# Performance work log

Hardware: AMD Instinct MI355X
Metric: run time of the kernel (lower is better)

## Reference

```python
import jax, jax.numpy as jnp
import numpy as np

B, N, C = 4, 32768, 3          # batch, proposals per sample, classes
PRE, POST = 4096, 512          # NMS_PRE_MAXSIZE, NMS_POST_MAXSIZE
THRESH = 0.7                   # NMS_THRESH


def setup_inputs() -> dict:
    key = jax.random.key(0)
    k1, k2, k3, k4 = jax.random.split(key, 4)
    # realistic 3D boxes: centers in a ~70m range, sizes 1-5m, heading in (-pi, pi)
    centers = jax.random.uniform(k1, (B, N, 3), minval=-35.0, maxval=35.0)
    sizes = jax.random.uniform(k2, (B, N, 3), minval=1.0, maxval=5.0)
    heading = jax.random.uniform(k3, (B, N, 1), minval=-np.pi, maxval=np.pi)
    batch_box_preds = jnp.concatenate([centers, sizes, heading], axis=-1)  # (B,N,7)
    batch_cls_preds = jax.random.normal(k4, (B, N, C))                     # (B,N,3)
    return {"batch_box_preds": batch_box_preds, "batch_cls_preds": batch_cls_preds}


def _bev_iou(boxes):
    # boxes: (K, 7) = (x, y, z, dx, dy, dz, ry); axis-aligned BEV IoU -> (K, K)
    x, y, dx, dy = boxes[:, 0], boxes[:, 1], boxes[:, 3], boxes[:, 4]
    x1, x2 = x - dx * 0.5, x + dx * 0.5
    y1, y2 = y - dy * 0.5, y + dy * 0.5
    iw = jnp.clip(jnp.minimum(x2[:, None], x2[None, :]) - jnp.maximum(x1[:, None], x1[None, :]), 0.0)
    ih = jnp.clip(jnp.minimum(y2[:, None], y2[None, :]) - jnp.maximum(y1[:, None], y1[None, :]), 0.0)
    inter = iw * ih
    area = dx * dy
    union = area[:, None] + area[None, :] - inter
    return inter / jnp.maximum(union, 1e-6)


def _nms_one(boxes, cls_preds):
    # boxes: (N, 7), cls_preds: (N, C)
    scores = jnp.max(cls_preds, axis=1)          # per-box max-class score
    labels = jnp.argmax(cls_preds, axis=1)
    top_scores, idx = jax.lax.top_k(scores, PRE)  # score-sorted candidates
    iou = _bev_iou(boxes[idx])                    # (PRE, PRE)
    ar = jnp.arange(PRE)

    def body(i, keep):
        # suppress later boxes overlapping a still-kept box i
        suppress = (iou[i] > THRESH) & keep[i] & (ar > i)
        return keep & (~suppress)

    keep = jax.lax.fori_loop(0, PRE, body, jnp.ones(PRE, dtype=bool))

    # take first POST kept (already score-ordered); pad with zeros like torch new_zeros buffers
    _, sel_local = jax.lax.top_k(jnp.where(keep, top_scores, -jnp.inf), POST)
    valid = keep[sel_local]
    sel = idx[sel_local]
    rois = jnp.where(valid[:, None], boxes[sel], 0.0)            # (POST, 7)
    roi_scores = jnp.where(valid, scores[sel], 0.0)              # (POST,)
    roi_labels = jnp.where(valid, labels[sel], 0) + 1            # (POST,), +1 as in proposal_layer
    return rois, roi_scores, roi_labels


def reference(batch_box_preds, batch_cls_preds):
    rois, roi_scores, roi_labels = jax.vmap(_nms_one)(batch_box_preds, batch_cls_preds)
    return rois, roi_scores, roi_labels
```

## Files before the change

### kernel.cpp

```cpp
#include <hip/hip_runtime.h>
#include <cstdint>
#include <cstddef>

#define BB 4
#define NN 32768
#define PRE 4096
#define POST 512
#define NW 64
#define PSEL 1024
#define PREF_CH 16

typedef unsigned long long u64;
typedef unsigned int u32;

#define SW(i) ((i) ^ (((i) >> 4) & 15))

__device__ __forceinline__ u32 enc_f32(float f) {
  u32 u = __float_as_uint(f);
  u32 m = (u32)((int)u >> 31) | 0x80000000u;
  return u ^ m;
}

__global__ void score_kernel(const float* __restrict__ cls,
                             float* __restrict__ scores, int* __restrict__ labels) {
  int g = blockIdx.x * blockDim.x + threadIdx.x;
  if (g >= BB * NN) return;
  const float* p = cls + (size_t)g * 3;
  float c0 = p[0], c1 = p[1], c2 = p[2];
  float m = c0; int l = 0;
  if (c1 > m) { m = c1; l = 1; }
  if (c2 > m) { m = c2; l = 2; }
  scores[g] = m;
  labels[g] = l;
}

template<int SELN, bool GATED>
__global__ __launch_bounds__(1024) void select_kernel_t(
    const float* __restrict__ scores, const float* __restrict__ boxes,
    const int* __restrict__ st_info,
    int* __restrict__ top_idx, float* __restrict__ top_score,
    float* __restrict__ bx1, float* __restrict__ bx2,
    float* __restrict__ by1, float* __restrict__ by2, float* __restrict__ bar) {
  constexpr bool HY = (SELN == PSEL);
  int b = blockIdx.x;
  if (GATED && st_info[b * 2 + 0] >= POST) return;
  int tid = threadIdx.x;
  int wv = tid >> 6;
  const float* sc = scores + (size_t)b * NN;

  __shared__ u32 hist16[16][256];
  __shared__ u32 sA[256], sB[256];
  __shared__ u32 scanbuf[1024];
  __shared__ u64 sortbuf[SELN];
  __shared__ u32 sh_prefix;
  __shared__ int sh_rem;

  const int e0 = tid * 32;
  u32 encs[32];
  {
    const float4* sc4 = (const float4*)(sc + e0);
#pragma unroll
    for (int k = 0; k < 8; ++k) {
      float4 v = sc4[k];
      encs[k * 4 + 0] = enc_f32(v.x);
      encs[k * 4 + 1] = enc_f32(v.y);
      encs[k * 4 + 2] = enc_f32(v.z);
      encs[k * 4 + 3] = enc_f32(v.w);
    }
  }

  u32 prefix = 0, known = 0;
  int remaining = SELN;
  for (int shift = 24; shift >= 0; shift -= 8) {
    for (int k = tid; k < 16 * 256; k += 1024) ((u32*)hist16)[k] = 0;
    __syncthreads();
#pragma unroll
    for (int k = 0; k < 32; ++k) {
      u32 u = encs[k];
      if ((u & known) == prefix) atomicAdd(&hist16[wv][(u >> shift) & 255u], 1u);
    }
    __syncthreads();
    if (tid < 256) {
      u32 t = 0;
#pragma unroll
      for (int w2 = 0; w2 < 16; ++w2) t += hist16[w2][tid];
      sA[tid] = t;
    }
    __syncthreads();
    u32* src = sA; u32* dst = sB;
    for (int off = 1; off < 256; off <<= 1) {
      if (tid < 256) dst[tid] = src[tid] + ((tid + off < 256) ? src[tid + off] : 0u);
      __syncthreads();
      u32* tp = src; src = dst; dst = tp;
    }
    if (tid < 256) {
      u32 sv = src[tid];
      u32 svn = (tid < 255) ? src[tid + 1] : 0u;
      if (sv >= (u32)remaining && svn < (u32)remaining) {
        sh_prefix = prefix | ((u32)tid << shift);
        sh_rem = remaining - (int)svn;
      }
    }
    __syncthreads();
    prefix = sh_prefix;
    remaining = sh_rem;
    known |= (0xFFu << shift);
    __syncthreads();
  }
  const u32 pivot = prefix;

  int gtc = 0, eqc = 0;
#pragma unroll
  for (int k = 0; k < 32; ++k) {
    gtc += (encs[k] > pivot);
    eqc += (encs[k] == pivot);
  }
  scanbuf[tid] = ((u32)gtc << 16) | (u32)eqc;
  __syncthreads();
  for (int off = 1; off < 1024; off <<= 1) {
    u32 v = scanbuf[tid];
    u32 add = (tid >= off) ? scanbuf[tid - off] : 0u;
    __syncthreads();
    scanbuf[tid] = v + add;
    __syncthreads();
  }
  u32 incl = scanbuf[tid];
  u32 totpk = scanbuf[1023];
  const int cnt_gt = (int)(totpk >> 16);
  int gt_base = (int)(incl >> 16) - gtc;
  int eq_base = (int)(incl & 0xFFFFu) - eqc;
  int gs = 0, es = 0;
#pragma unroll
  for (int k = 0; k < 32; ++k) {
    u32 u = encs[k];
    int e = e0 + k;
    u64 key = ((u64)u << 32) | (u32)(~(u32)e);
    if (u > pivot) {
      int pos = gt_base + (gs++);
      sortbuf[HY ? pos : SW(pos)] = key;
    } else if (u == pivot) {
      int g = eq_base + (es++);
      if (g < remaining) {
        int pos = cnt_gt + g;
        sortbuf[HY ? pos : SW(pos)] = key;
      }
    }
  }
  __syncthreads();

  if constexpr (HY) {
    u64 key = sortbuf[tid];
#pragma unroll
    for (int k2 = 2; k2 <= 64; k2 <<= 1) {
      for (int j = k2 >> 1; j > 0; j >>= 1) {
        u64 o = __shfl_xor(key, j, 64);
        bool take_max = (((tid & k2) == 0) == ((tid & j) == 0));
        key = ((key > o) == take_max) ? key : o;
      }
    }
    for (int k2 = 128; k2 <= PSEL; k2 <<= 1) {
      for (int j = k2 >> 1; j >= 64; j >>= 1) {
        __syncthreads();
        sortbuf[tid] = key;
        __syncthreads();
        u64 o = sortbuf[tid ^ j];
        bool take_max = (((tid & k2) == 0) == ((tid & j) == 0));
        key = ((key > o) == take_max) ? key : o;
      }
      for (int j = 32; j > 0; j >>= 1) {
        u64 o = __shfl_xor(key, j, 64);
        bool take_max = (((tid & k2) == 0) == ((tid & j) == 0));
        key = ((key > o) == take_max) ? key : o;
      }
    }
    {
#pragma clang fp contract(off)
      int e = (int)(~(u32)(key & 0xFFFFFFFFull));
      top_idx[b * PRE + tid] = e;
      top_score[b * PRE + tid] = sc[e];
      const float* bx = boxes + ((size_t)b * NN + e) * 7;
      float x = bx[0], y = bx[1], dx = bx[3], dy = bx[4];
      float hx = dx * 0.5f, hy = dy * 0.5f;
      bx1[b * PRE + tid] = x - hx;
      bx2[b * PRE + tid] = x + hx;
      by1[b * PRE + tid] = y - hy;
      by2[b * PRE + tid] = y + hy;
      bar[b * PRE + tid] = dx * dy;
    }
  } else {
    for (int k = 2; k <= SELN; k <<= 1) {
      for (int j = k >> 1; j > 0; j >>= 1) {
        for (int p = tid; p < SELN / 2; p += 1024) {
          int low = p & (j - 1);
          int i = ((p ^ low) << 1) | low;
          int ixj = i + j;
          u64 a = sortbuf[SW(i)], c = sortbuf[SW(ixj)];
          bool desc = ((i & k) == 0);
          if (desc ? (a < c) : (a > c)) { sortbuf[SW(i)] = c; sortbuf[SW(ixj)] = a; }
        }
        __syncthreads();
      }
    }
    {
#pragma clang fp contract(off)
      for (int s = tid; s < SELN; s += 1024) {
        u64 key = sortbuf[SW(s)];
        int e = (int)(~(u32)(key & 0xFFFFFFFFull));
        top_idx[b * PRE + s] = e;
        top_score[b * PRE + s] = sc[e];
        const float* bx = boxes + ((size_t)b * NN + e) * 7;
        float x = bx[0], y = bx[1], dx = bx[3], dy = bx[4];
        float hx = dx * 0.5f, hy = dy * 0.5f;
        bx1[b * PRE + s] = x - hx;
        bx2[b * PRE + s] = x + hx;
        by1[b * PRE + s] = y - hy;
        by2[b * PRE + s] = y + hy;
        bar[b * PRE + s] = dx * dy;
      }
    }
  }
}

__device__ __forceinline__ void mask_tile(
    const float* __restrict__ bx1, const float* __restrict__ bx2,
    const float* __restrict__ by1, const float* __restrict__ by2,
    const float* __restrict__ bar, u64* __restrict__ mask,
    int b, int rb, int cb, int t) {
#pragma clang fp contract(off)
  int i = rb * 64 + t;
  int j0 = cb * 64 + t;
  float cx1 = bx1[b * PRE + j0], cx2 = bx2[b * PRE + j0];
  float cy1 = by1[b * PRE + j0], cy2 = by2[b * PRE + j0];
  float car = bar[b * PRE + j0];
  float ix1 = bx1[b * PRE + i], ix2 = bx2[b * PRE + i];
  float iy1 = by1[b * PRE + i], iy2 = by2[b * PRE + i];
  float ia = bar[b * PRE + i];
  u64 bits = 0ull;
  int jbase = cb * 64;
  for (int jj = 0; jj < 64; ++jj) {
    float jx1 = __shfl(cx1, jj, 64);
    float jx2 = __shfl(cx2, jj, 64);
    float jy1 = __shfl(cy1, jj, 64);
    float jy2 = __shfl(cy2, jj, 64);
    float jar = __shfl(car, jj, 64);
    if (jbase + jj > i) {
      float iw = fminf(ix2, jx2) - fmaxf(ix1, jx1);
      iw = fmaxf(iw, 0.0f);
      float ih = fminf(iy2, jy2) - fmaxf(iy1, jy1);
      ih = fmaxf(ih, 0.0f);
      float inter = iw * ih;
      float uni = ia + jar - inter;
      float iou = inter / fmaxf(uni, 1e-6f);
      if (iou > 0.7f) bits |= (1ull << jj);
    }
  }
  mask[((size_t)b * PRE + i) * NW + cb] = bits;
}

__global__ void mask_prefix_kernel(const float* __restrict__ bx1, const float* __restrict__ bx2,
                                   const float* __restrict__ by1, const float* __restrict__ by2,
                                   const float* __restrict__ bar, u64* __restrict__ mask) {
  int cb = blockIdx.x, rb = blockIdx.y, b = blockIdx.z;
  if (cb < rb) return;
  mask_tile(bx1, bx2, by1, by2, bar, mask, b, rb, cb, threadIdx.x);
}

__global__ __launch_bounds__(256) void mask_full_kernel(
    const float* __restrict__ bx1, const float* __restrict__ bx2,
    const float* __restrict__ by1, const float* __restrict__ by2,
    const float* __restrict__ bar, u64* __restrict__ mask,
    const int* __restrict__ st_info) {
  int b = blockIdx.z;
  if (st_info[b * 2 + 0] >= POST) return;
  int rb = blockIdx.y;
  int cb = blockIdx.x * 4 + (threadIdx.x >> 6);
  if (cb < rb) return;
  mask_tile(bx1, bx2, by1, by2, bar, mask, b, rb, cb, threadIdx.x & 63);
}

template<bool FULL>
__global__ __launch_bounds__(256) void nms_kernel_t(
    const u64* __restrict__ mask, u64* __restrict__ keep_words,
    int* __restrict__ st_info) {
  int b = blockIdx.x;
  if (FULL && st_info[b * 2 + 0] >= POST) return;
  int tid = threadIdx.x;
  int lane = tid & 63;
  int wv = tid >> 6;
  __shared__ u64 part[2][4][64];

  const u64* base = mask + (size_t)b * PRE * NW;
  u64 rem = 0ull, keepw = 0ull;
  int kept = 0;
  const int c1 = FULL ? NW : PREF_CH;

  int c = 0;
  while (c < c1) {
    u64 remc = __shfl(rem, c, 64);
    const u64* rowp = base + ((size_t)(c * 64 + wv * 16)) * NW + lane;
    u64 m[16];
#pragma unroll
    for (int k = 0; k < 16; ++k) m[k] = rowp[(size_t)k * NW];
    u64 dg = base[((size_t)(c * 64 + lane)) * NW + c];
    u64 nz = __ballot(dg != 0ull);
    while (nz) {
      int i2 = __builtin_ctzll(nz);
      nz &= nz - 1ull;
      u64 di = __shfl(dg, i2, 64);
      if (!((remc >> i2) & 1ull)) remc |= di;
    }
    u64 K = ~remc;
    if (lane == c) keepw = K;
    kept += __popcll(K);

    u32 kb = (u32)((K >> (wv * 16)) & 0xFFFFull);
    u64 acc = 0ull;
#pragma unroll
    for (int k = 0; k < 16; ++k)
      if ((kb >> k) & 1u) acc |= m[k];
    part[c & 1][wv][lane] = acc;
    __syncthreads();
    rem |= part[c & 1][0][lane] | part[c & 1][1][lane] |
           part[c & 1][2][lane] | part[c & 1][3][lane];
    ++c;
    if (kept >= POST) break;
  }

  if (wv == 0) {
    keep_words[b * 64 + lane] = keepw;
    if (!FULL && lane == 0) st_info[b * 2 + 0] = kept;
  }
}

__global__ __launch_bounds__(1024) void output_kernel(
    const u64* __restrict__ keep_words, const int* __restrict__ top_idx,
    const float* __restrict__ top_score, const int* __restrict__ labels,
    const float* __restrict__ boxes, float* __restrict__ out) {
  int b = blockIdx.x, tid = threadIdx.x;
  __shared__ u32 scanbuf[1024];
  __shared__ int sh_total;

  u64 w = keep_words[b * 64 + (tid >> 4)];
  u32 my4 = (u32)((w >> ((tid & 15) * 4)) & 0xFull);
  int cnt = __popc(my4);
  scanbuf[tid] = (u32)cnt;
  __syncthreads();
  for (int off = 1; off < 1024; off <<= 1) {
    u32 v = scanbuf[tid];
    u32 add = (tid >= off) ? scanbuf[tid - off] : 0u;
    __syncthreads();
    scanbuf[tid] = v + add;
    __syncthreads();
  }
  int base = (int)scanbuf[tid] - cnt;
  if (tid == 1023) sh_total = (int)scanbuf[1023];
  __syncthreads();
  int total = sh_total;

  float* rois = out;
  float* rsc = out + BB * POST * 7;
  float* rlb = rsc + BB * POST;

  int r = 0;
  for (int k = 0; k < 4; ++k) {
    if ((my4 >> k) & 1u) {
      int rank = base + (r++);
      if (rank < POST) {
        int i = tid * 4 + k;
        int idx = top_idx[b * PRE + i];
        const float* bx = boxes + ((size_t)b * NN + idx) * 7;
        float* ro = rois + ((size_t)b * POST + rank) * 7;
        for (int c = 0; c < 7; ++c) ro[c] = bx[c];
        rsc[b * POST + rank] = top_score[b * PRE + i];
        rlb[b * POST + rank] = (float)(labels[b * NN + idx] + 1);
      }
    }
  }
  for (int s = tid; s < POST; s += 1024) {
    if (s >= total) {
      float* ro = rois + ((size_t)b * POST + s) * 7;
      for (int c = 0; c < 7; ++c) ro[c] = 0.0f;
      rsc[b * POST + s] = 0.0f;
      rlb[b * POST + s] = 1.0f;
    }
  }
}

extern "C" void kernel_launch(void* const* d_in, const int* in_sizes, int n_in,
                              void* d_out, int out_size, void* d_ws, size_t ws_size,
                              hipStream_t stream) {
  const float* boxes = (const float*)d_in[0];
  const float* cls = (const float*)d_in[1];
  float* out = (float*)d_out;

  char* w = (char*)d_ws;
  float* scores = (float*)w;    w += (size_t)BB * NN * 4;
  int* labels = (int*)w;        w += (size_t)BB * NN * 4;
  int* top_idx = (int*)w;       w += (size_t)BB * PRE * 4;
  float* top_score = (float*)w; w += (size_t)BB * PRE * 4;
  float* bx1 = (float*)w;       w += (size_t)BB * PRE * 4;
  float* bx2 = (float*)w;       w += (size_t)BB * PRE * 4;
  float* by1 = (float*)w;       w += (size_t)BB * PRE * 4;
  float* by2 = (float*)w;       w += (size_t)BB * PRE * 4;
  float* bar = (float*)w;       w += (size_t)BB * PRE * 4;
  u64* mask = (u64*)w;          w += (size_t)BB * PRE * NW * 8;
  u64* keepw = (u64*)w;         w += (size_t)BB * 64 * 8;
  int* st_info = (int*)w;       w += (size_t)BB * 2 * 4;

  score_kernel<<<(BB * NN + 255) / 256, 256, 0, stream>>>(cls, scores, labels);
  select_kernel_t<PSEL, false><<<BB, 1024, 0, stream>>>(
      scores, boxes, st_info, top_idx, top_score, bx1, bx2, by1, by2, bar);
  mask_prefix_kernel<<<dim3(PREF_CH, PREF_CH, BB), 64, 0, stream>>>(
      bx1, bx2, by1, by2, bar, mask);
  nms_kernel_t<false><<<BB, 256, 0, stream>>>(mask, keepw, st_info);
  select_kernel_t<PRE, true><<<BB, 1024, 0, stream>>>(
      scores, boxes, st_info, top_idx, top_score, bx1, bx2, by1, by2, bar);
  mask_full_kernel<<<dim3(NW / 4, NW, BB), 256, 0, stream>>>(
      bx1, bx2, by1, by2, bar, mask, st_info);
  nms_kernel_t<true><<<BB, 256, 0, stream>>>(mask, keepw, st_info);
  output_kernel<<<BB, 1024, 0, stream>>>(keepw, top_idx, top_score, labels, boxes, out);
}
```

Measured before the change: 134.4 us.

## Split top-1024 selection into multi-block histogram, pivot, compact and sort kernels

Replaces the per-batch single-block radix select for the first 1024 candidates with a pipeline. A 64-block prep kernel fuses score/label computation with a 4096-bin histogram, a pivot kernel finds the threshold bin, and a multi-block compact kernel gathers candidates using warp scans and global atomics. A 1024-thread kernel then resolves ties by rank counting and runs the bitonic sort. The aim is to spread the full 32768-element scan across many CUs instead of four blocks, at the cost of extra launches and a rank step that is quadratic in the size of the pivot bin.

Measured after the change: 148.7 us. 1.11x slower.

```diff
diff --git a/kernel.cpp b/kernel.cpp
--- a/kernel.cpp
+++ b/kernel.cpp
@@ -9,6 +9,8 @@
 #define NW 64
 #define PSEL 1024
 #define PREF_CH 16
+#define NBIN 4096
+#define CEQ 32768
 
 typedef unsigned long long u64;
 typedef unsigned int u32;
@@ -21,17 +23,199 @@
   return u ^ m;
 }
 
-__global__ void score_kernel(const float* __restrict__ cls,
-                             float* __restrict__ scores, int* __restrict__ labels) {
-  int g = blockIdx.x * blockDim.x + threadIdx.x;
-  if (g >= BB * NN) return;
-  const float* p = cls + (size_t)g * 3;
-  float c0 = p[0], c1 = p[1], c2 = p[2];
-  float m = c0; int l = 0;
-  if (c1 > m) { m = c1; l = 1; }
-  if (c2 > m) { m = c2; l = 2; }
-  scores[g] = m;
-  labels[g] = l;
+__global__ __launch_bounds__(256) void prep_kernel(
+    const float* __restrict__ cls, float* __restrict__ scores,
+    int* __restrict__ labels, u32* __restrict__ bhist) {
+  int blk = blockIdx.x, b = blockIdx.y;
+  int tid = threadIdx.x;
+  __shared__ u32 lhist[NBIN];
+  for (int i = tid; i < NBIN; i += 256) lhist[i] = 0;
+  __syncthreads();
+
+  const int E = blk * 2048 + tid * 8;
+  const float4* cp4 = (const float4*)(cls + ((size_t)b * NN + E) * 3);
+  float4 v0 = cp4[0], v1 = cp4[1], v2 = cp4[2], v3 = cp4[3], v4 = cp4[4], v5 = cp4[5];
+  float fa[24] = {v0.x, v0.y, v0.z, v0.w, v1.x, v1.y, v1.z, v1.w,
+                  v2.x, v2.y, v2.z, v2.w, v3.x, v3.y, v3.z, v3.w,
+                  v4.x, v4.y, v4.z, v4.w, v5.x, v5.y, v5.z, v5.w};
+  float sc8[8];
+  int lb8[8];
+#pragma unroll
+  for (int k = 0; k < 8; ++k) {
+    float c0 = fa[3 * k], c1 = fa[3 * k + 1], c2 = fa[3 * k + 2];
+    float m = c0; int l = 0;
+    if (c1 > m) { m = c1; l = 1; }
+    if (c2 > m) { m = c2; l = 2; }
+    sc8[k] = m;
+    lb8[k] = l;
+    atomicAdd(&lhist[enc_f32(m) >> 20], 1u);
+  }
+  float4* so = (float4*)(scores + (size_t)b * NN + E);
+  so[0] = make_float4(sc8[0], sc8[1], sc8[2], sc8[3]);
+  so[1] = make_float4(sc8[4], sc8[5], sc8[6], sc8[7]);
+  int4* lo = (int4*)(labels + (size_t)b * NN + E);
+  lo[0] = make_int4(lb8[0], lb8[1], lb8[2], lb8[3]);
+  lo[1] = make_int4(lb8[4], lb8[5], lb8[6], lb8[7]);
+  __syncthreads();
+  u32* row = bhist + (size_t)(b * 16 + blk) * NBIN;
+  for (int i = tid; i < NBIN; i += 256) row[i] = lhist[i];
+}
+
+__global__ __launch_bounds__(256) void pivot_kernel(
+    const u32* __restrict__ bhist, int* __restrict__ st2, u32* __restrict__ gcnt) {
+  int b = blockIdx.x, t = threadIdx.x;
+  u32 sb[16];
+#pragma unroll
+  for (int j = 0; j < 16; ++j) {
+    u32 s = 0;
+#pragma unroll
+    for (int k = 0; k < 16; ++k) s += bhist[(size_t)(b * 16 + k) * NBIN + t * 16 + j];
+    sb[j] = s;
+  }
+  u32 T = 0;
+#pragma unroll
+  for (int j = 0; j < 16; ++j) T += sb[j];
+  __shared__ u32 ssum[256];
+  ssum[t] = T;
+  __syncthreads();
+  for (int off = 1; off < 256; off <<= 1) {
+    u32 v = ssum[t];
+    u32 a = (t + off < 256) ? ssum[t + off] : 0u;
+    __syncthreads();
+    ssum[t] = v + a;
+    __syncthreads();
+  }
+  u32 cum = (t < 255) ? ssum[t + 1] : 0u;
+  for (int j = 15; j >= 0; --j) {
+    u32 incl = cum + sb[j];
+    if (incl >= (u32)PSEL && cum < (u32)PSEL) {
+      st2[b * 2 + 0] = t * 16 + j;
+      st2[b * 2 + 1] = PSEL - (int)cum;
+    }
+    cum = incl;
+  }
+  if (t == 0) { gcnt[b * 2 + 0] = 0; gcnt[b * 2 + 1] = 0; }
+}
+
+__global__ __launch_bounds__(256) void compact_kernel(
+    const float* __restrict__ scores, const int* __restrict__ st2,
+    u32* __restrict__ gcnt, u64* __restrict__ cand, u64* __restrict__ ceq) {
+  int blk = blockIdx.x, b = blockIdx.y;
+  int tid = threadIdx.x, lane = tid & 63;
+  const int E = blk * 2048 + tid * 8;
+  const float4* s4 = (const float4*)(scores + (size_t)b * NN + E);
+  float4 a = s4[0], c = s4[1];
+  float fs[8] = {a.x, a.y, a.z, a.w, c.x, c.y, c.z, c.w};
+  const u32 pb = (u32)st2[b * 2 + 0];
+  u32 encs[8];
+  u32 gbits = 0, ebits = 0;
+  u32 gtl = 0, eql = 0;
+#pragma unroll
+  for (int k = 0; k < 8; ++k) {
+    u32 u = enc_f32(fs[k]);
+    encs[k] = u;
+    u32 bin = u >> 20;
+    if (bin > pb) { gbits |= 1u << k; gtl++; }
+    else if (bin == pb) { ebits |= 1u << k; eql++; }
+  }
+  u64 pack = ((u64)gtl << 32) | eql;
+#pragma unroll
+  for (int off = 1; off < 64; off <<= 1) {
+    u64 t = __shfl_up(pack, off, 64);
+    if (lane >= off) pack += t;
+  }
+  u64 tot = __shfl(pack, 63, 64);
+  u32 bg = 0, be = 0;
+  if (lane == 63) {
+    bg = atomicAdd(&gcnt[b * 2 + 0], (u32)(tot >> 32));
+    be = atomicAdd(&gcnt[b * 2 + 1], (u32)(tot & 0xFFFFFFFFu));
+  }
+  bg = (u32)__shfl((int)bg, 63, 64);
+  be = (u32)__shfl((int)be, 63, 64);
+  int pg = (int)(bg + (u32)(pack >> 32) - gtl);
+  int pe = (int)(be + (u32)(pack & 0xFFFFFFFFu) - eql);
+#pragma unroll
+  for (int k = 0; k < 8; ++k) {
+    u64 key = ((u64)encs[k] << 32) | (u32)(~(u32)(E + k));
+    if ((gbits >> k) & 1u) cand[(size_t)b * PSEL + (pg++)] = key;
+    else if ((ebits >> k) & 1u) ceq[(size_t)b * CEQ + (pe++)] = key;
+  }
+}
+
+__global__ __launch_bounds__(1024) void sort1024_kernel(
+    const float* __restrict__ scores, const float* __restrict__ boxes,
+    const int* __restrict__ st2, const u32* __restrict__ gcnt,
+    const u64* __restrict__ cand, const u64* __restrict__ ceq,
+    int* __restrict__ top_idx, float* __restrict__ top_score,
+    float* __restrict__ bx1, float* __restrict__ bx2,
+    float* __restrict__ by1, float* __restrict__ by2, float* __restrict__ bar) {
+  int b = blockIdx.x;
+  int tid = threadIdx.x;
+  const float* sc = scores + (size_t)b * NN;
+  __shared__ u64 sortbuf[PSEL];
+  __shared__ u64 ebuf[2048];
+
+  const int g = (int)gcnt[b * 2 + 0];
+  const int m = (int)gcnt[b * 2 + 1];
+  const int need = st2[b * 2 + 1];
+
+  if (tid < g) sortbuf[tid] = cand[(size_t)b * PSEL + tid];
+
+  const int qmax = (m + 1023) >> 10;
+  for (int q = 0; q < qmax; ++q) {
+    int i = q * 1024 + tid;
+    u64 kk = (i < m) ? ceq[(size_t)b * CEQ + i] : 0ull;
+    u32 rr = 0;
+    for (int base = 0; base < m; base += 2048) {
+      int cn = min(2048, m - base);
+      __syncthreads();
+      for (int k = tid; k < cn; k += 1024) ebuf[k] = ceq[(size_t)b * CEQ + base + k];
+      __syncthreads();
+      for (int j = 0; j < cn; ++j) rr += (ebuf[j] > kk);
+    }
+    if (i < m && rr < (u32)need) sortbuf[g + rr] = kk;
+  }
+  __syncthreads();
+
+  u64 key = sortbuf[tid];
+#pragma unroll
+  for (int k2 = 2; k2 <= 64; k2 <<= 1) {
+    for (int j = k2 >> 1; j > 0; j >>= 1) {
+      u64 o = __shfl_xor(key, j, 64);
+      bool take_max = (((tid & k2) == 0) == ((tid & j) == 0));
+      key = ((key > o) == take_max) ? key : o;
+    }
+  }
+  for (int k2 = 128; k2 <= PSEL; k2 <<= 1) {
+    for (int j = k2 >> 1; j >= 64; j >>= 1) {
+      __syncthreads();
+      sortbuf[tid] = key;
+      __syncthreads();
+      u64 o = sortbuf[tid ^ j];
+      bool take_max = (((tid & k2) == 0) == ((tid & j) == 0));
+      key = ((key > o) == take_max) ? key : o;
+    }
+    for (int j = 32; j > 0; j >>= 1) {
+      u64 o = __shfl_xor(key, j, 64);
+      bool take_max = (((tid & k2) == 0) == ((tid & j) == 0));
+      key = ((key > o) == take_max) ? key : o;
+    }
+  }
+
+  {
+#pragma clang fp contract(off)
+    int e = (int)(~(u32)(key & 0xFFFFFFFFull));
+    top_idx[b * PRE + tid] = e;
+    top_score[b * PRE + tid] = sc[e];
+    const float* bx = boxes + ((size_t)b * NN + e) * 7;
+    float x = bx[0], y = bx[1], dx = bx[3], dy = bx[4];
+    float hx = dx * 0.5f, hy = dy * 0.5f;
+    bx1[b * PRE + tid] = x - hx;
+    bx2[b * PRE + tid] = x + hx;
+    by1[b * PRE + tid] = y - hy;
+    by2[b * PRE + tid] = y + hy;
+    bar[b * PRE + tid] = dx * dy;
+  }
 }
 
 template<int SELN, bool GATED>
@@ -41,7 +225,6 @@
     int* __restrict__ top_idx, float* __restrict__ top_score,
     float* __restrict__ bx1, float* __restrict__ bx2,
     float* __restrict__ by1, float* __restrict__ by2, float* __restrict__ bar) {
-  constexpr bool HY = (SELN == PSEL);
   int b = blockIdx.x;
   if (GATED && st_info[b * 2 + 0] >= POST) return;
   int tid = threadIdx.x;
@@ -136,87 +319,42 @@
     int e = e0 + k;
     u64 key = ((u64)u << 32) | (u32)(~(u32)e);
     if (u > pivot) {
-      int pos = gt_base + (gs++);
-      sortbuf[HY ? pos : SW(pos)] = key;
+      sortbuf[SW(gt_base + gs)] = key; gs++;
     } else if (u == pivot) {
       int g = eq_base + (es++);
-      if (g < remaining) {
-        int pos = cnt_gt + g;
-        sortbuf[HY ? pos : SW(pos)] = key;
+      if (g < remaining) sortbuf[SW(cnt_gt + g)] = key;
+    }
+  }
+  __syncthreads();
+
+  for (int k = 2; k <= SELN; k <<= 1) {
+    for (int j = k >> 1; j > 0; j >>= 1) {
+      for (int p = tid; p < SELN / 2; p += 1024) {
+        int low = p & (j - 1);
+        int i = ((p ^ low) << 1) | low;
+        int ixj = i + j;
+        u64 a = sortbuf[SW(i)], c = sortbuf[SW(ixj)];
+        bool desc = ((i & k) == 0);
+        if (desc ? (a < c) : (a > c)) { sortbuf[SW(i)] = c; sortbuf[SW(ixj)] = a; }
       }
-    }
-  }
-  __syncthreads();
-
-  if constexpr (HY) {
-    u64 key = sortbuf[tid];
-#pragma unroll
-    for (int k2 = 2; k2 <= 64; k2 <<= 1) {
-      for (int j = k2 >> 1; j > 0; j >>= 1) {
-        u64 o = __shfl_xor(key, j, 64);
-        bool take_max = (((tid & k2) == 0) == ((tid & j) == 0));
-        key = ((key > o) == take_max) ? key : o;
-      }
-    }
-    for (int k2 = 128; k2 <= PSEL; k2 <<= 1) {
-      for (int j = k2 >> 1; j >= 64; j >>= 1) {
-        __syncthreads();
-        sortbuf[tid] = key;
-        __syncthreads();
-        u64 o = sortbuf[tid ^ j];
-        bool take_max = (((tid & k2) == 0) == ((tid & j) == 0));
-        key = ((key > o) == take_max) ? key : o;
-      }
-      for (int j = 32; j > 0; j >>= 1) {
-        u64 o = __shfl_xor(key, j, 64);
-        bool take_max = (((tid & k2) == 0) == ((tid & j) == 0));
-        key = ((key > o) == take_max) ? key : o;
-      }
-    }
-    {
+      __syncthreads();
+    }
+  }
+  {
 #pragma clang fp contract(off)
+    for (int s = tid; s < SELN; s += 1024) {
+      u64 key = sortbuf[SW(s)];
       int e = (int)(~(u32)(key & 0xFFFFFFFFull));
-      top_idx[b * PRE + tid] = e;
-      top_score[b * PRE + tid] = sc[e];
+      top_idx[b * PRE + s] = e;
+      top_score[b * PRE + s] = sc[e];
       const float* bx = boxes + ((size_t)b * NN + e) * 7;
       float x = bx[0], y = bx[1], dx = bx[3], dy = bx[4];
       float hx = dx * 0.5f, hy = dy * 0.5f;
-      bx1[b * PRE + tid] = x - hx;
-      bx2[b * PRE + tid] = x + hx;
-      by1[b * PRE + tid] = y - hy;
-      by2[b * PRE + tid] = y + hy;
-      bar[b * PRE + tid] = dx * dy;
-    }
-  } else {
-    for (int k = 2; k <= SELN; k <<= 1) {
-      for (int j = k >> 1; j > 0; j >>= 1) {
-        for (int p = tid; p < SELN / 2; p += 1024) {
-          int low = p & (j - 1);
-          int i = ((p ^ low) << 1) | low;
-          int ixj = i + j;
-          u64 a = sortbuf[SW(i)], c = sortbuf[SW(ixj)];
-          bool desc = ((i & k) == 0);
-          if (desc ? (a < c) : (a > c)) { sortbuf[SW(i)] = c; sortbuf[SW(ixj)] = a; }
-        }
-        __syncthreads();
-      }
-    }
-    {
-#pragma clang fp contract(off)
-      for (int s = tid; s < SELN; s += 1024) {
-        u64 key = sortbuf[SW(s)];
-        int e = (int)(~(u32)(key & 0xFFFFFFFFull));
-        top_idx[b * PRE + s] = e;
-        top_score[b * PRE + s] = sc[e];
-        const float* bx = boxes + ((size_t)b * NN + e) * 7;
-        float x = bx[0], y = bx[1], dx = bx[3], dy = bx[4];
-        float hx = dx * 0.5f, hy = dy * 0.5f;
-        bx1[b * PRE + s] = x - hx;
-        bx2[b * PRE + s] = x + hx;
-        by1[b * PRE + s] = y - hy;
-        by2[b * PRE + s] = y + hy;
-        bar[b * PRE + s] = dx * dy;
-      }
+      bx1[b * PRE + s] = x - hx;
+      bx2[b * PRE + s] = x + hx;
+      by1[b * PRE + s] = y - hy;
+      by2[b * PRE + s] = y + hy;
+      bar[b * PRE + s] = dx * dy;
     }
   }
 }
@@ -406,10 +544,17 @@
   u64* mask = (u64*)w;          w += (size_t)BB * PRE * NW * 8;
   u64* keepw = (u64*)w;         w += (size_t)BB * 64 * 8;
   int* st_info = (int*)w;       w += (size_t)BB * 2 * 4;
-
-  score_kernel<<<(BB * NN + 255) / 256, 256, 0, stream>>>(cls, scores, labels);
-  select_kernel_t<PSEL, false><<<BB, 1024, 0, stream>>>(
-      scores, boxes, st_info, top_idx, top_score, bx1, bx2, by1, by2, bar);
+  u32* bhist = (u32*)w;         w += (size_t)BB * 16 * NBIN * 4;
+  u64* cand = (u64*)w;          w += (size_t)BB * PSEL * 8;
+  u64* ceq = (u64*)w;           w += (size_t)BB * CEQ * 8;
+  int* st2 = (int*)w;           w += (size_t)BB * 2 * 4;
+  u32* gcnt = (u32*)w;          w += (size_t)BB * 2 * 4;
+
+  prep_kernel<<<dim3(16, BB), 256, 0, stream>>>(cls, scores, labels, bhist);
+  pivot_kernel<<<BB, 256, 0, stream>>>(bhist, st2, gcnt);
+  compact_kernel<<<dim3(16, BB), 256, 0, stream>>>(scores, st2, gcnt, cand, ceq);
+  sort1024_kernel<<<BB, 1024, 0, stream>>>(scores, boxes, st2, gcnt, cand, ceq,
+                                           top_idx, top_score, bx1, bx2, by1, by2, bar);
   mask_prefix_kernel<<<dim3(PREF_CH, PREF_CH, BB), 64, 0, stream>>>(
       bx1, bx2, by1, by2, bar, mask);
   nms_kernel_t<false><<<BB, 256, 0, stream>>>(mask, keepw, st_info);
```
